# Optimization experiments

Hardware: AMD Instinct MI355X
Metric: run time of the kernel (lower is better)

Reference implementation:

```python
import jax, jax.numpy as jnp
import numpy as np

B, L, D, H = 2, 2048, 2048, 16
C = D // H  # head dim = 128
EPS = 1e-5


def setup_inputs() -> dict:
    key = jax.random.key(0)
    k1, k2, k3, k4 = jax.random.split(key, 4)
    scale = 1.0 / np.sqrt(D)
    return {
        "x": jax.random.normal(k1, (B, L, D), dtype=jnp.float32),
        "theta": jax.random.uniform(k2, (B, L, D // 2), dtype=jnp.float32) * 6.2831853,
        "w_qkv": jax.random.normal(k3, (3 * D, D), dtype=jnp.float32) * scale,
        "w_y": jax.random.normal(k4, (D, D), dtype=jnp.float32) * scale,
        "b_y": jnp.zeros((D,), dtype=jnp.float32),
    }


def _rms_norm(t):
    # RMSNorm over last dim, eps=1e-5, no affine
    return t * jax.lax.rsqrt(jnp.mean(t * t, axis=-1, keepdims=True) + EPS)


def _apply_rope(q, k, theta):
    # q, k: (B, H, L, C); theta: (B, H, L, C//2)
    qr, qi = q[..., 0::2], q[..., 1::2]
    kr, ki = k[..., 0::2], k[..., 1::2]
    cos_t, sin_t = jnp.cos(theta), jnp.sin(theta)
    q_rot = jnp.stack((qr * cos_t - qi * sin_t, qr * sin_t + qi * cos_t), axis=-1).reshape(q.shape)
    k_rot = jnp.stack((kr * cos_t - ki * sin_t, kr * sin_t + ki * cos_t), axis=-1).reshape(k.shape)
    return q_rot, k_rot


def reference(x, theta, w_qkv, w_y, b_y):
    # QKV projection: (B, L, 3D)
    qkv = jnp.einsum("bld,ed->ble", x, w_qkv)
    # rearrange '... L (n H C) -> n ... H L C'
    qkv = qkv.reshape(B, L, 3, H, C).transpose(2, 0, 3, 1, 4)  # (3, B, H, L, C)
    q, k, v = qkv[0], qkv[1], qkv[2]
    q, k = _rms_norm(q), _rms_norm(k)
    # theta: (B, L, H*C/2) -> (B, H, L, C/2)
    th = theta.reshape(B, L, H, C // 2).transpose(0, 2, 1, 3)
    q, k = _apply_rope(q, k, th)
    # scaled dot-product attention
    scores = jnp.einsum("bhqc,bhkc->bhqk", q, k) / np.sqrt(C).astype(np.float32)
    attn = jax.nn.softmax(scores, axis=-1)
    y = jnp.einsum("bhqk,bhkc->bhqc", attn, v)
    # (B, H, L, C) -> (B, L, H*C)
    y = y.transpose(0, 2, 1, 3).reshape(B, L, D)
    return jnp.einsum("bld,ed->ble", y, w_y) + b_y
```

## Files before the change

### kernel.cpp

```cpp
#include <hip/hip_runtime.h>
#include <stdint.h>

typedef uint16_t u16;
typedef __attribute__((ext_vector_type(8))) short bf16x8;
typedef __attribute__((ext_vector_type(4))) float f32x4;


__device__ __forceinline__ u16 f2bf(float f) {
  uint32_t u = __builtin_bit_cast(uint32_t, f);
  u += 0x7fffu + ((u >> 16) & 1u);
  return (u16)(u >> 16);
}
__device__ __forceinline__ float bf2f(u16 h) {
  return __builtin_bit_cast(float, (uint32_t)h << 16);
}
__device__ __forceinline__ uint32_t pack2bf(float a, float b) {
  uint32_t ua = __builtin_bit_cast(uint32_t, a) + 0x7fffu;
  uint32_t ub = __builtin_bit_cast(uint32_t, b) + 0x7fffu;
  return (ua >> 16) | (ub & 0xffff0000u);
}
__device__ __forceinline__ void gl_lds16(const u16* g, u16* l) {
  __builtin_amdgcn_global_load_lds((const __attribute__((address_space(1))) uint32_t*)g,
                                   (__attribute__((address_space(3))) uint32_t*)l, 16, 0, 0);
}

__global__ __launch_bounds__(256) void castk(const float* __restrict__ in,
                                             u16* __restrict__ out, int n) {
  int idx = (blockIdx.x * 256 + threadIdx.x) * 4;
  int stride = gridDim.x * 256 * 4;
  for (int i = idx; i < n; i += stride) {
    float4 v = *(const float4*)(in + i);
    uint32_t lo = (uint32_t)f2bf(v.x) | ((uint32_t)f2bf(v.y) << 16);
    uint32_t hi = (uint32_t)f2bf(v.z) | ((uint32_t)f2bf(v.w) << 16);
    *(uint2*)(out + i) = make_uint2(lo, hi);
  }
}

__global__ __launch_bounds__(512, 1) void gemm8_qkv(
    const u16* __restrict__ A, const u16* __restrict__ Bw,
    u16* __restrict__ qb, u16* __restrict__ kb, u16* __restrict__ vt) {
  __shared__ u16 sm[57344];
  const int K = 2048;
  const int tid = threadIdx.x, lane = tid & 63;
  const int wid = tid >> 6, g = lane >> 4, lr = lane & 15;
  const int wm = wid >> 2, wn = wid & 3;
  const int f = blockIdx.x;
  const int xc = f & 7, rr = f >> 3;
  const int by = rr & 15, bx = xc * 4 + (rr >> 4);
  const int m0 = by * 256, n0 = bx * 192;
  const int srow = tid >> 3, sjs = (tid & 7) ^ (srow & 7);

  auto stA = [&](int buf, int kt, int R) {
    gl_lds16(A + (size_t)(m0 + R + srow) * K + kt * 64 + sjs * 8,
             &sm[buf * 28672 + R * 64 + tid * 8]);
  };
  auto stB = [&](int buf, int kt, int R) {
    gl_lds16(Bw + (size_t)(n0 + R + srow) * K + kt * 64 + sjs * 8,
             &sm[buf * 28672 + 16384 + R * 64 + tid * 8]);
  };
  auto rdA = [&](const u16* As, int mf, int ks) {
    int ra = wm * 128 + mf * 16 + lr;
    return *(const bf16x8*)&As[ra * 64 + (((ks * 4 + g) ^ (ra & 7)) * 8)];
  };
  auto rdB = [&](const u16* Bs, int nf, int ks) {
    int rb = wn * 48 + nf * 16 + lr;
    return *(const bf16x8*)&Bs[rb * 64 + (((ks * 4 + g) ^ (rb & 7)) * 8)];
  };

  f32x4 acc[8][3] = {};
  bf16x8 bc[3][2], fP0[4][2], fP1[4][2];

  stB(0, 0, 0); stB(0, 0, 64); stB(0, 0, 128);
  stA(0, 0, 0); stA(0, 0, 128);
  stA(0, 0, 64); stA(0, 0, 192);
  asm volatile("s_waitcnt vmcnt(2)" ::: "memory");
  __builtin_amdgcn_s_barrier();
  {
    const u16* As0 = &sm[0];
#pragma unroll
    for (int i = 0; i < 4; ++i)
#pragma unroll
      for (int ks = 0; ks < 2; ++ks) fP0[i][ks] = rdA(As0, i, ks);
  }

  for (int t = 0; t < 32; ++t) {
    const int cur = t & 1, nxt = cur ^ 1;
    const int kn = (t < 31) ? t + 1 : 31;
    const u16* Asc = &sm[cur * 28672];
    const u16* Bsc = &sm[cur * 28672 + 16384];
    const u16* Asn = &sm[nxt * 28672];

    stB(nxt, kn, 0); stB(nxt, kn, 64); stB(nxt, kn, 128);
    stA(nxt, kn, 0); stA(nxt, kn, 128);
    asm volatile("s_waitcnt vmcnt(5)" ::: "memory");
    __builtin_amdgcn_s_barrier();
#pragma unroll
    for (int nf = 0; nf < 3; ++nf)
#pragma unroll
      for (int ks = 0; ks < 2; ++ks) bc[nf][ks] = rdB(Bsc, nf, ks);
#pragma unroll
    for (int i = 0; i < 4; ++i)
#pragma unroll
      for (int ks = 0; ks < 2; ++ks) fP1[i][ks] = rdA(Asc, 4 + i, ks);
    __builtin_amdgcn_s_setprio(1);
#pragma unroll
    for (int i = 0; i < 4; ++i)
#pragma unroll
      for (int nf = 0; nf < 3; ++nf) {
        acc[i][nf] = __builtin_amdgcn_mfma_f32_16x16x32_bf16(
            fP0[i][0], bc[nf][0], acc[i][nf], 0, 0, 0);
        acc[i][nf] = __builtin_amdgcn_mfma_f32_16x16x32_bf16(
            fP0[i][1], bc[nf][1], acc[i][nf], 0, 0, 0);
      }
    __builtin_amdgcn_s_setprio(0);

    stA(nxt, kn, 64); stA(nxt, kn, 192);
    asm volatile("s_waitcnt vmcnt(2)" ::: "memory");
    __builtin_amdgcn_s_barrier();
#pragma unroll
    for (int i = 0; i < 4; ++i)
#pragma unroll
      for (int ks = 0; ks < 2; ++ks) fP0[i][ks] = rdA(Asn, i, ks);
    __builtin_amdgcn_s_setprio(1);
#pragma unroll
    for (int i = 0; i < 4; ++i)
#pragma unroll
      for (int nf = 0; nf < 3; ++nf) {
        acc[4 + i][nf] = __builtin_amdgcn_mfma_f32_16x16x32_bf16(
            fP1[i][0], bc[nf][0], acc[4 + i][nf], 0, 0, 0);
        acc[4 + i][nf] = __builtin_amdgcn_mfma_f32_16x16x32_bf16(
            fP1[i][1], bc[nf][1], acc[4 + i][nf], 0, 0, 0);
      }
    __builtin_amdgcn_s_setprio(0);
  }
  asm volatile("s_waitcnt vmcnt(0)" ::: "memory");

#pragma unroll
  for (int mf = 0; mf < 8; ++mf)
#pragma unroll
    for (int nf = 0; nf < 3; ++nf) {
      int n = n0 + wn * 48 + nf * 16 + lr;
      int s = n >> 11, h = (n >> 7) & 15, cb = n & 127;
#pragma unroll
      for (int r = 0; r < 4; ++r) {
        int m = m0 + wm * 128 + mf * 16 + g * 4 + r;
        int b = m >> 11, lp = m & 2047;
        u16 val = f2bf(acc[mf][nf][r]);
        if (s == 0)
          qb[(size_t)((b * 16 + h) * 2048 + lp) * 128 + cb] = val;
        else if (s == 1)
          kb[(size_t)((b * 16 + h) * 2048 + lp) * 128 + cb] = val;
        else
          vt[(size_t)((b * 16 + h) * 128 + cb) * 2048 + lp] = val;
      }
    }
}

__global__ __launch_bounds__(256) void gemm_out(
    const u16* __restrict__ A, const u16* __restrict__ Bw, int K,
    float* __restrict__ out, const float* __restrict__ bias) {
  __shared__ u16 As[128 * 64];
  __shared__ u16 Bs[128 * 64];
  const int tid = threadIdx.x;
  const int lane = tid & 63, wid = tid >> 6;
  const int g = lane >> 4, lr = lane & 15;
  const int wm = wid >> 1, wn = wid & 1;
  const int m0 = blockIdx.y * 128, n0 = blockIdx.x * 128;
  f32x4 acc[4][4] = {};
  const int nk = K >> 6;
  for (int kt = 0; kt < nk; ++kt) {
    const int kbase = kt * 64;
#pragma unroll
    for (int i = 0; i < 4; ++i) {
      int ci = wid * 256 + i * 64 + lane;
      int row = ci >> 3, j = ci & 7;
      int js = j ^ (row & 7);
      gl_lds16(A + (size_t)(m0 + row) * K + kbase + js * 8, &As[(wid * 256 + i * 64) * 8]);
    }
#pragma unroll
    for (int i = 0; i < 4; ++i) {
      int ci = wid * 256 + i * 64 + lane;
      int row = ci >> 3, j = ci & 7;
      int js = j ^ (row & 7);
      gl_lds16(Bw + (size_t)(n0 + row) * K + kbase + js * 8, &Bs[(wid * 256 + i * 64) * 8]);
    }
    __syncthreads();
#pragma unroll
    for (int ks = 0; ks < 2; ++ks) {
      bf16x8 af[4], bfr[4];
#pragma unroll
      for (int t = 0; t < 4; ++t) {
        int ra = wm * 64 + t * 16 + lr;
        af[t] = *(const bf16x8*)&As[ra * 64 + (((ks * 4 + g) ^ (ra & 7)) * 8)];
        int rb = wn * 64 + t * 16 + lr;
        bfr[t] = *(const bf16x8*)&Bs[rb * 64 + (((ks * 4 + g) ^ (rb & 7)) * 8)];
      }
#pragma unroll
      for (int mt = 0; mt < 4; ++mt)
#pragma unroll
        for (int nt = 0; nt < 4; ++nt)
          acc[mt][nt] =
              __builtin_amdgcn_mfma_f32_16x16x32_bf16(af[mt], bfr[nt], acc[mt][nt], 0, 0, 0);
    }
    __syncthreads();
  }
#pragma unroll
  for (int mt = 0; mt < 4; ++mt)
#pragma unroll
    for (int nt = 0; nt < 4; ++nt) {
      int n = n0 + wn * 64 + nt * 16 + lr;
      float bv = bias[n];
#pragma unroll
      for (int r = 0; r < 4; ++r) {
        int m = m0 + wm * 64 + mt * 16 + g * 4 + r;
        out[(size_t)m * 2048 + n] = acc[mt][nt][r] + bv;
      }
    }
}

__global__ __launch_bounds__(256) void qk_fix(u16* __restrict__ qb, u16* __restrict__ kb,
                                              const float* __restrict__ theta) {
  const int row = blockIdx.x * 4 + (threadIdx.x >> 6);
  const int lane = threadIdx.x & 63;
  const int bh = row >> 11, l = row & 2047;
  const int b = bh >> 4, h = bh & 15;
  float th = theta[(size_t)(b * 2048 + l) * 1024 + h * 64 + lane];
  float sn, cs;
  __sincosf(th, &sn, &cs);
#pragma unroll
  for (int which = 0; which < 2; ++which) {
    u16* buf = which ? kb : qb;
    uint32_t* p = (uint32_t*)(buf + (size_t)row * 128) + lane;
    uint32_t v = *p;
    float x0 = bf2f((u16)(v & 0xffff)), x1 = bf2f((u16)(v >> 16));
    float ss = x0 * x0 + x1 * x1;
#pragma unroll
    for (int m = 1; m <= 32; m <<= 1) ss += __shfl_xor(ss, m);
    float rn = rsqrtf(ss * (1.0f / 128.0f) + 1e-5f);
    if (which == 0) rn *= 0.12751743f;
    x0 *= rn;
    x1 *= rn;
    float y0 = x0 * cs - x1 * sn;
    float y1 = x0 * sn + x1 * cs;
    *p = (uint32_t)f2bf(y0) | ((uint32_t)f2bf(y1) << 16);
  }
}

__global__ __launch_bounds__(256, 2) void attn_k(const u16* __restrict__ qb,
                                                 const u16* __restrict__ kb,
                                                 const u16* __restrict__ vt,
                                                 u16* __restrict__ yb) {
  __shared__ u16 sm[32768];
  const int gid = blockIdx.x;
  const int slot = gid & 7, rest = gid >> 3;
  const int bh = slot * 4 + (rest & 3);
  const int qtile = rest >> 2;
  const int b = bh >> 4, h = bh & 15;
  const int tid = threadIdx.x, lane = tid & 63, wid = tid >> 6;
  const int g = lane >> 4, lr = lane & 15;
  const int q0 = qtile * 128 + wid * 32;

  bf16x8 qf[2][4];
#pragma unroll
  for (int qs = 0; qs < 2; ++qs) {
    const u16* qrow = qb + (size_t)(bh * 2048 + q0 + qs * 16 + lr) * 128;
#pragma unroll
    for (int ks = 0; ks < 4; ++ks) qf[qs][ks] = *(const bf16x8*)&qrow[ks * 32 + g * 8];
  }

  auto stage = [&](int buf, int kv) {
#pragma unroll
    for (int i = 0; i < 2; ++i) {
      int ci = i * 256 + tid;
      int row = ci >> 4, j = ci & 15;
      gl_lds16(kb + (size_t)(bh * 2048 + kv + row) * 128 + (j ^ (row & 7)) * 8,
               &sm[buf * 8192 + ci * 8]);
    }
#pragma unroll
    for (int i = 2; i < 4; ++i) {
      int ci = (i - 2) * 256 + tid;
      int row = ci >> 4, j = ci & 15;
      gl_lds16(kb + (size_t)(bh * 2048 + kv + 32 + row) * 128 + (j ^ (row & 7)) * 8,
               &sm[buf * 8192 + 4096 + ci * 8]);
    }
#pragma unroll
    for (int i = 0; i < 4; ++i) {
      int ci = i * 256 + tid;
      int row = ci >> 3, j = ci & 7;
      gl_lds16(vt + (size_t)(bh * 128 + row) * 2048 + kv + (j ^ (row & 7)) * 8,
               &sm[16384 + buf * 8192 + ci * 8]);
    }
  };

  f32x4 acc[2][8] = {};
  float mrun[2] = {-1e30f, -1e30f}, lrun[2] = {0.f, 0.f};
  const int sA = (2 * (g & 1)) * 16 + lr, sB = sA + 16;
  const bool hi2 = (g >> 1) != 0;

  stage(0, 0);
  asm volatile("s_waitcnt vmcnt(0)" ::: "memory");
  __builtin_amdgcn_s_barrier();

  for (int t = 0; t < 32; ++t) {
    const int cur = t & 1;
    if (t < 31) stage(cur ^ 1, (t + 1) * 64);
    const u16* Ks = &sm[cur * 8192];
    const u16* Vs = &sm[16384 + cur * 8192];

    f32x4 st[2][4] = {};
#pragma unroll
    for (int ks = 0; ks < 4; ++ks) {
      bf16x8 kf[4];
#pragma unroll
      for (int kt = 0; kt < 4; ++kt) {
        int row = kt * 16 + lr;
        kf[kt] = *(const bf16x8*)&Ks[row * 128 + (((ks * 4 + g) ^ (row & 7)) * 8)];
      }
#pragma unroll
      for (int kt = 0; kt < 4; ++kt)
#pragma unroll
        for (int qs = 0; qs < 2; ++qs)
          st[qs][kt] =
              __builtin_amdgcn_mfma_f32_16x16x32_bf16(kf[kt], qf[qs][ks], st[qs][kt], 0, 0, 0);
    }

    float pmax[2];
#pragma unroll
    for (int qs = 0; qs < 2; ++qs) {
      float m01 = fmaxf(fmaxf(st[qs][0][0], st[qs][0][1]), fmaxf(st[qs][0][2], st[qs][0][3]));
      float m23 = fmaxf(fmaxf(st[qs][1][0], st[qs][1][1]), fmaxf(st[qs][1][2], st[qs][1][3]));
      float m45 = fmaxf(fmaxf(st[qs][2][0], st[qs][2][1]), fmaxf(st[qs][2][2], st[qs][2][3]));
      float m67 = fmaxf(fmaxf(st[qs][3][0], st[qs][3][1]), fmaxf(st[qs][3][2], st[qs][3][3]));
      float mx = fmaxf(fmaxf(m01, m23), fmaxf(m45, m67));
      mx = fmaxf(mx, __shfl_xor(mx, 16));
      mx = fmaxf(mx, __shfl_xor(mx, 32));
      pmax[qs] = mx;
    }
    float need = fmaxf(pmax[0] - mrun[0], pmax[1] - mrun[1]);
    if (!__all(need <= 8.0f)) {
#pragma unroll
      for (int qs = 0; qs < 2; ++qs) {
        float mnew = fmaxf(mrun[qs], pmax[qs]);
        float corr = __builtin_amdgcn_exp2f(mrun[qs] - mnew);
        lrun[qs] *= corr;
        mrun[qs] = mnew;
#pragma unroll
        for (int ct = 0; ct < 8; ++ct) {
          acc[qs][ct][0] *= corr;
          acc[qs][ct][1] *= corr;
          acc[qs][ct][2] *= corr;
          acc[qs][ct][3] *= corr;
        }
      }
    }
    uint32_t pw[2][4][2];
#pragma unroll
    for (int qs = 0; qs < 2; ++qs) {
      float rsum = 0.f;
#pragma unroll
      for (int kt = 0; kt < 4; ++kt)
#pragma unroll
        for (int hf = 0; hf < 2; ++hf) {
          float e0 = __builtin_amdgcn_exp2f(st[qs][kt][2 * hf] - mrun[qs]);
          float e1 = __builtin_amdgcn_exp2f(st[qs][kt][2 * hf + 1] - mrun[qs]);
          rsum += e0 + e1;
          pw[qs][kt][hf] = pack2bf(e0, e1);
        }
      rsum += __shfl_xor(rsum, 16);
      rsum += __shfl_xor(rsum, 32);
      lrun[qs] += rsum;
    }

#pragma unroll
    for (int ks2 = 0; ks2 < 2; ++ks2) {
      bf16x8 pf[2];
#pragma unroll
      for (int qs = 0; qs < 2; ++qs) {
        uint32_t a0 = __shfl(pw[qs][ks2 * 2][0], sA);
        uint32_t a1 = __shfl(pw[qs][ks2 * 2][1], sA);
        uint32_t a2 = __shfl(pw[qs][ks2 * 2][0], sB);
        uint32_t a3 = __shfl(pw[qs][ks2 * 2][1], sB);
        uint32_t b0 = __shfl(pw[qs][ks2 * 2 + 1][0], sA);
        uint32_t b1 = __shfl(pw[qs][ks2 * 2 + 1][1], sA);
        uint32_t b2 = __shfl(pw[qs][ks2 * 2 + 1][0], sB);
        uint32_t b3 = __shfl(pw[qs][ks2 * 2 + 1][1], sB);
        union {
          uint32_t u[4];
          bf16x8 v;
        } tt;
        tt.u[0] = hi2 ? b0 : a0;
        tt.u[1] = hi2 ? b1 : a1;
        tt.u[2] = hi2 ? b2 : a2;
        tt.u[3] = hi2 ? b3 : a3;
        pf[qs] = tt.v;
      }
#pragma unroll
      for (int ct = 0; ct < 8; ++ct) {
        int row = ct * 16 + lr;
        bf16x8 vf = *(const bf16x8*)&Vs[row * 64 + (((ks2 * 4 + g) ^ (row & 7)) * 8)];
#pragma unroll
        for (int qs = 0; qs < 2; ++qs)
          acc[qs][ct] = __builtin_amdgcn_mfma_f32_16x16x32_bf16(vf, pf[qs], acc[qs][ct], 0, 0, 0);
      }
    }
    if (t < 31) {
      asm volatile("s_waitcnt vmcnt(0)" ::: "memory");
      __builtin_amdgcn_s_barrier();
    }
  }

#pragma unroll
  for (int qs = 0; qs < 2; ++qs) {
    float inv = 1.f / lrun[qs];
    const size_t orow = (size_t)(b * 2048 + q0 + qs * 16 + lr) * 2048 + h * 128;
#pragma unroll
    for (int ct = 0; ct < 8; ++ct) {
      uint32_t lo = pack2bf(acc[qs][ct][0] * inv, acc[qs][ct][1] * inv);
      uint32_t hi = pack2bf(acc[qs][ct][2] * inv, acc[qs][ct][3] * inv);
      *(uint2*)&yb[orow + ct * 16 + g * 4] = make_uint2(lo, hi);
    }
  }
}

extern "C" void kernel_launch(void* const* d_in, const int* in_sizes, int n_in,
                              void* d_out, int out_size, void* d_ws, size_t ws_size,
                              hipStream_t stream) {
  const float* x = (const float*)d_in[0];
  const float* theta = (const float*)d_in[1];
  const float* wqkv = (const float*)d_in[2];
  const float* wy = (const float*)d_in[3];
  const float* by = (const float*)d_in[4];
  float* out = (float*)d_out;
  char* ws = (char*)d_ws;
  u16* xb  = (u16*)(ws + 0);
  u16* wqb = (u16*)(ws + 16777216);
  u16* wyb = (u16*)(ws + 41943040);
  u16* qb  = (u16*)(ws + 50331648);
  u16* kb  = (u16*)(ws + 67108864);
  u16* vt  = (u16*)(ws + 83886080);
  u16* yb  = (u16*)(ws + 100663296);

  castk<<<2048, 256, 0, stream>>>(x, xb, 2 * 2048 * 2048);
  castk<<<2048, 256, 0, stream>>>(wqkv, wqb, 3 * 2048 * 2048);
  castk<<<1024, 256, 0, stream>>>(wy, wyb, 2048 * 2048);

  gemm8_qkv<<<512, 512, 0, stream>>>(xb, wqb, qb, kb, vt);
  qk_fix<<<16384, 256, 0, stream>>>(qb, kb, theta);
  attn_k<<<512, 256, 0, stream>>>(qb, kb, vt, yb);
  gemm_out<<<dim3(16, 32), 256, 0, stream>>>(yb, wyb, 2048, out, by);
}
```

Baseline: 303.3 us.

## Deepen QKV GEMM prefetch to two tiles ahead and drop swizzled block mapping

The QKV GEMM now prefetches global tiles two K-steps ahead into the buffer it has just finished reading, instead of one step ahead into the other buffer. It adds explicit lgkmcnt waits and sched_barriers around the MFMA blocks, and replaces the XCD-aware swizzled block index with a plain 2D grid. The attention K staging loop is also simplified, which keeps the same addresses. The goal is to hide more global load latency in the GEMM. The risks are extra barriers per iteration and possibly worse L2 locality without the swizzle.

After: 309.3 us. Within noise of the previous version (+2.0%).

```diff
diff --git a/kernel.cpp b/kernel.cpp
--- a/kernel.cpp
+++ b/kernel.cpp
@@ -44,10 +44,7 @@
   const int tid = threadIdx.x, lane = tid & 63;
   const int wid = tid >> 6, g = lane >> 4, lr = lane & 15;
   const int wm = wid >> 2, wn = wid & 3;
-  const int f = blockIdx.x;
-  const int xc = f & 7, rr = f >> 3;
-  const int by = rr & 15, bx = xc * 4 + (rr >> 4);
-  const int m0 = by * 256, n0 = bx * 192;
+  const int m0 = blockIdx.y * 256, n0 = blockIdx.x * 192;
   const int srow = tid >> 3, sjs = (tid & 7) ^ (srow & 7);
 
   auto stA = [&](int buf, int kt, int R) {
@@ -68,70 +65,74 @@
   };
 
   f32x4 acc[8][3] = {};
-  bf16x8 bc[3][2], fP0[4][2], fP1[4][2];
-
-  stB(0, 0, 0); stB(0, 0, 64); stB(0, 0, 128);
+  bf16x8 bc[3][2], fLo[4][2], fHi[4][2];
+
   stA(0, 0, 0); stA(0, 0, 128);
-  stA(0, 0, 64); stA(0, 0, 192);
-  asm volatile("s_waitcnt vmcnt(2)" ::: "memory");
+  stB(0, 0, 0); stB(0, 0, 64); stB(0, 0, 128); stA(0, 0, 64); stA(0, 0, 192);
+  stA(1, 1, 0); stA(1, 1, 128);
+  stB(1, 1, 0); stB(1, 1, 64); stB(1, 1, 128); stA(1, 1, 64); stA(1, 1, 192);
+  asm volatile("s_waitcnt vmcnt(7)" ::: "memory");
   __builtin_amdgcn_s_barrier();
-  {
-    const u16* As0 = &sm[0];
-#pragma unroll
-    for (int i = 0; i < 4; ++i)
-#pragma unroll
-      for (int ks = 0; ks < 2; ++ks) fP0[i][ks] = rdA(As0, i, ks);
-  }
+#pragma unroll
+  for (int i = 0; i < 4; ++i)
+#pragma unroll
+    for (int ks = 0; ks < 2; ++ks) fLo[i][ks] = rdA(&sm[0], i, ks);
 
   for (int t = 0; t < 32; ++t) {
     const int cur = t & 1, nxt = cur ^ 1;
-    const int kn = (t < 31) ? t + 1 : 31;
+    const int kn = (t < 30) ? t + 2 : 31;
     const u16* Asc = &sm[cur * 28672];
     const u16* Bsc = &sm[cur * 28672 + 16384];
     const u16* Asn = &sm[nxt * 28672];
 
-    stB(nxt, kn, 0); stB(nxt, kn, 64); stB(nxt, kn, 128);
-    stA(nxt, kn, 0); stA(nxt, kn, 128);
-    asm volatile("s_waitcnt vmcnt(5)" ::: "memory");
+#pragma unroll
+    for (int nf = 0; nf < 3; ++nf)
+#pragma unroll
+      for (int ks = 0; ks < 2; ++ks) bc[nf][ks] = rdB(Bsc, nf, ks);
+#pragma unroll
+    for (int i = 0; i < 4; ++i)
+#pragma unroll
+      for (int ks = 0; ks < 2; ++ks) fHi[i][ks] = rdA(Asc, 4 + i, ks);
+    stA(cur, kn, 0); stA(cur, kn, 128);
     __builtin_amdgcn_s_barrier();
-#pragma unroll
-    for (int nf = 0; nf < 3; ++nf)
-#pragma unroll
-      for (int ks = 0; ks < 2; ++ks) bc[nf][ks] = rdB(Bsc, nf, ks);
-#pragma unroll
-    for (int i = 0; i < 4; ++i)
-#pragma unroll
-      for (int ks = 0; ks < 2; ++ks) fP1[i][ks] = rdA(Asc, 4 + i, ks);
+    asm volatile("s_waitcnt lgkmcnt(0)" ::: "memory");
+    __builtin_amdgcn_sched_barrier(0);
     __builtin_amdgcn_s_setprio(1);
 #pragma unroll
     for (int i = 0; i < 4; ++i)
 #pragma unroll
       for (int nf = 0; nf < 3; ++nf) {
         acc[i][nf] = __builtin_amdgcn_mfma_f32_16x16x32_bf16(
-            fP0[i][0], bc[nf][0], acc[i][nf], 0, 0, 0);
+            fLo[i][0], bc[nf][0], acc[i][nf], 0, 0, 0);
         acc[i][nf] = __builtin_amdgcn_mfma_f32_16x16x32_bf16(
-            fP0[i][1], bc[nf][1], acc[i][nf], 0, 0, 0);
+            fLo[i][1], bc[nf][1], acc[i][nf], 0, 0, 0);
       }
     __builtin_amdgcn_s_setprio(0);
-
-    stA(nxt, kn, 64); stA(nxt, kn, 192);
-    asm volatile("s_waitcnt vmcnt(2)" ::: "memory");
+    asm volatile("s_waitcnt vmcnt(7)" ::: "memory");
     __builtin_amdgcn_s_barrier();
+
 #pragma unroll
     for (int i = 0; i < 4; ++i)
 #pragma unroll
-      for (int ks = 0; ks < 2; ++ks) fP0[i][ks] = rdA(Asn, i, ks);
+      for (int ks = 0; ks < 2; ++ks) fLo[i][ks] = rdA(Asn, i, ks);
+    stB(cur, kn, 0); stB(cur, kn, 64); stB(cur, kn, 128);
+    stA(cur, kn, 64); stA(cur, kn, 192);
+    __builtin_amdgcn_s_barrier();
+    asm volatile("s_waitcnt lgkmcnt(0)" ::: "memory");
+    __builtin_amdgcn_sched_barrier(0);
     __builtin_amdgcn_s_setprio(1);
 #pragma unroll
     for (int i = 0; i < 4; ++i)
 #pragma unroll
       for (int nf = 0; nf < 3; ++nf) {
         acc[4 + i][nf] = __builtin_amdgcn_mfma_f32_16x16x32_bf16(
-            fP1[i][0], bc[nf][0], acc[4 + i][nf], 0, 0, 0);
+            fHi[i][0], bc[nf][0], acc[4 + i][nf], 0, 0, 0);
         acc[4 + i][nf] = __builtin_amdgcn_mfma_f32_16x16x32_bf16(
-            fP1[i][1], bc[nf][1], acc[4 + i][nf], 0, 0, 0);
+            fHi[i][1], bc[nf][1], acc[4 + i][nf], 0, 0, 0);
       }
     __builtin_amdgcn_s_setprio(0);
+    asm volatile("s_waitcnt vmcnt(7)" ::: "memory");
+    __builtin_amdgcn_s_barrier();
   }
   asm volatile("s_waitcnt vmcnt(0)" ::: "memory");
 
@@ -270,18 +271,11 @@
 
   auto stage = [&](int buf, int kv) {
 #pragma unroll
-    for (int i = 0; i < 2; ++i) {
+    for (int i = 0; i < 4; ++i) {
       int ci = i * 256 + tid;
       int row = ci >> 4, j = ci & 15;
       gl_lds16(kb + (size_t)(bh * 2048 + kv + row) * 128 + (j ^ (row & 7)) * 8,
                &sm[buf * 8192 + ci * 8]);
-    }
-#pragma unroll
-    for (int i = 2; i < 4; ++i) {
-      int ci = (i - 2) * 256 + tid;
-      int row = ci >> 4, j = ci & 15;
-      gl_lds16(kb + (size_t)(bh * 2048 + kv + 32 + row) * 128 + (j ^ (row & 7)) * 8,
-               &sm[buf * 8192 + 4096 + ci * 8]);
     }
 #pragma unroll
     for (int i = 0; i < 4; ++i) {
@@ -444,7 +438,7 @@
   castk<<<2048, 256, 0, stream>>>(wqkv, wqb, 3 * 2048 * 2048);
   castk<<<1024, 256, 0, stream>>>(wy, wyb, 2048 * 2048);
 
-  gemm8_qkv<<<512, 512, 0, stream>>>(xb, wqb, qb, kb, vt);
+  gemm8_qkv<<<dim3(32, 16), 512, 0, stream>>>(xb, wqb, qb, kb, vt);
   qk_fix<<<16384, 256, 0, stream>>>(qb, kb, theta);
   attn_k<<<512, 256, 0, stream>>>(qb, kb, vt, yb);
   gemm_out<<<dim3(16, 32), 256, 0, stream>>>(yb, wyb, 2048, out, by);
```
